# Kernel tuning notes

Hardware: AMD Instinct MI355X
Metric: run time of the kernel (lower is better)

## Reference

```python
import math
import jax, jax.numpy as jnp
import numpy as np

RESO = 64
RADIUS = 1.3
EMB_DIM = 64
NUM_EMB = 512
COMMIT = 0.25
NFP = 4
NFD = 4
SH_DEG = 2
B = 256
_UNITS = 2.0 * RADIUS / (RESO - 1)
STEP = _UNITS / 8.0                      # calc_step_size with factor 4
NINT = int(math.sqrt(3.0) * 2.0 * RADIUS / STEP) - 1   # 871
NSH = (SH_DEG + 1) ** 2                  # 9
MLP_IN = EMB_DIM + 6 * (NFP + NFD)       # 112
MLP_H = 32
MLP_OUT = NSH * 3 + 1                    # 28


def _eval_sh(d):
    # real SH basis, degree 2 -> 9 coeffs, evaluated on unit directions [B,3]
    x, y, z = d[:, 0], d[:, 1], d[:, 2]
    C0 = 0.28209479177387814
    C1 = 0.4886025119029199
    C20, C22, C24 = 1.0925484305920792, 0.31539156525252005, 0.5462742152960396
    return jnp.stack([
        jnp.full_like(x, C0), -C1 * y, C1 * z, -C1 * x,
        C20 * x * y, -C20 * y * z, C22 * (2 * z * z - x * x - y * y),
        -C20 * x * z, C24 * (x * x - y * y)], axis=-1)


def _pe(x, nf):
    # NeRF positional encoding: [N,3] -> [N, 6*nf]
    freqs = (2.0 ** jnp.arange(nf)).astype(x.dtype)
    ang = x[..., None] * freqs                              # [N,3,nf]
    return jnp.concatenate([jnp.sin(ang), jnp.cos(ang)], axis=-1).reshape(x.shape[0], 6 * nf)


def _forward(rays_o, rays_d, data, emb_w, W1, b1, W2, b2, W3, b3):
    rd = rays_d / jnp.linalg.norm(rays_d, axis=1, keepdims=True)
    # ray/AABB intersection, uniform marching (get_intersections)
    inv = 1.0 / rd
    t1 = (-RADIUS - rays_o) * inv
    t2 = (RADIUS - rays_o) * inv
    tnear = jnp.maximum(jnp.max(jnp.minimum(t1, t2), axis=1), 0.0)
    ts = tnear[:, None] + STEP * jnp.arange(NINT, dtype=rays_o.dtype)[None, :]  # [B,NINT]
    pts = rays_o[:, None, :] + ts[..., None] * rd[:, None, :]                   # [B,NINT,3]
    mask = jnp.all(jnp.abs(pts) < RADIUS, axis=-1)                              # [B,NINT]
    pf = pts.reshape(-1, 3)                                                     # [N,3]
    mf = mask.reshape(-1).astype(pf.dtype)                                      # [N]

    # fetch_coarse_interp: trilinear gather from [C,D,H,W] grid (align_corners)
    p = pf / RADIUS
    idx = jnp.clip((p + 1.0) * 0.5 * (RESO - 1), 0.0, RESO - 1)
    i0 = jnp.floor(idx).astype(jnp.int32)
    fr = idx - i0
    i1 = jnp.minimum(i0 + 1, RESO - 1)
    dT = jnp.transpose(data, (1, 2, 3, 0))  # [D,H,W,C]
    g = lambda iz, iy, ix: dT[iz, iy, ix]   # [N,C] gather
    x0, y0, z0 = i0[:, 0], i0[:, 1], i0[:, 2]
    x1, y1, z1 = i1[:, 0], i1[:, 1], i1[:, 2]
    wx, wy, wz = fr[:, 0:1], fr[:, 1:2], fr[:, 2:3]
    c00 = g(z0, y0, x0) * (1 - wx) + g(z0, y0, x1) * wx
    c01 = g(z0, y1, x0) * (1 - wx) + g(z0, y1, x1) * wx
    c10 = g(z1, y0, x0) * (1 - wx) + g(z1, y0, x1) * wx
    c11 = g(z1, y1, x0) * (1 - wx) + g(z1, y1, x1) * wx
    coarse = (c00 * (1 - wy) + c01 * wy) * (1 - wz) + (c10 * (1 - wy) + c11 * wy) * wz  # [N,C]

    # VectorQuantizerEMA forward (outputs are pre-EMA-update, identical in train/eval)
    d2 = (jnp.sum(coarse * coarse, axis=1, keepdims=True)
          + jnp.sum(emb_w * emb_w, axis=1) - 2.0 * coarse @ emb_w.T)  # [N,K]
    code = jnp.argmin(d2, axis=1)
    quant = emb_w[code]                                               # [N,C]
    cnt = jnp.maximum(jnp.sum(mf), 1.0)
    e_loss = jnp.sum(mf[:, None] * (jax.lax.stop_gradient(quant) - coarse) ** 2) / (cnt * EMB_DIM)
    loss = COMMIT * e_loss
    quant_st = coarse + jax.lax.stop_gradient(quant - coarse)
    counts = jax.ops.segment_sum(mf, code, num_segments=NUM_EMB)
    avg = counts / cnt
    perplexity = jnp.exp(-jnp.sum(avg * jnp.log(avg + 1e-10)))

    # world2finecoo + positional encoding
    pcc = pf * (RESO / (2.0 * RADIUS)) + RESO / 2.0
    fine = (pcc - jnp.floor(pcc)) * 2.0 - 1.0
    dirs = jnp.broadcast_to(rd[:, None, :], pts.shape).reshape(-1, 3)
    pe = jnp.concatenate([_pe(fine, NFP), _pe(dirs, NFD)], axis=1)    # [N,48]

    # fine MLP
    h = jax.nn.relu(jnp.concatenate([quant_st, pe], axis=1) @ W1 + b1)
    h = jax.nn.relu(h @ W2 + b2)
    shd = h @ W3 + b3                                                 # [N,28]

    # render: sigma2alpha + SH -> rgb + compositing (masked-out points get 0 weight)
    sigma = (jax.nn.relu(shd[:, -1]) * mf).reshape(B, NINT)
    alpha = 1.0 - jnp.exp(-sigma * STEP)
    Tc = jnp.cumprod(1.0 - alpha + 1e-10, axis=1)
    T = jnp.concatenate([jnp.ones((B, 1), alpha.dtype), Tc[:, :-1]], axis=1)
    w = alpha * T                                                     # abs_light [B,NINT]
    shm = _eval_sh(rd)                                                # [B,9]
    shrgb = shd[:, :-1].reshape(-1, 3, NSH)
    shm_f = jnp.broadcast_to(shm[:, None, :], (B, NINT, NSH)).reshape(-1, NSH)
    rgb_pt = (jnp.sum(shm_f[:, None, :] * shrgb, axis=-1) * mf[:, None]).reshape(B, NINT, 3)
    rgb_pt = jnp.clip(rgb_pt + 0.5, 0.0, 1.0)                         # shrgb2rgb per-sample
    rgb = jnp.sum(w[..., None] * rgb_pt, axis=1) + (1.0 - jnp.sum(w, axis=1, keepdims=True))
    depth = jnp.sum(w * ts, axis=1)
    return rgb, depth, loss, perplexity


def setup_inputs() -> dict:
    key = jax.random.key(0)
    ks = jax.random.split(key, 8)
    rays_o = (jax.random.uniform(ks[0], (B, 3)) * 2.0 - 1.0) * 0.3
    rays_d = jax.random.normal(ks[1], (B, 3))
    data = jax.random.normal(ks[2], (EMB_DIM, RESO, RESO, RESO)) * 0.1
    emb_w = jax.random.normal(ks[3], (NUM_EMB, EMB_DIM))
    W1 = jax.random.normal(ks[4], (MLP_IN, MLP_H)) * (1.0 / math.sqrt(MLP_IN))
    W2 = jax.random.normal(ks[5], (MLP_H, MLP_H)) * (1.0 / math.sqrt(MLP_H))
    W3 = jax.random.normal(ks[6], (MLP_H, MLP_OUT)) * (1.0 / math.sqrt(MLP_H))
    return {
        'rays_o': rays_o, 'rays_d': rays_d, 'grid_id': 0,
        'data': data, 'emb_w': emb_w,
        'W1': W1, 'b1': jnp.zeros((MLP_H,)),
        'W2': W2, 'b2': jnp.zeros((MLP_H,)),
        'W3': W3, 'b3': jnp.zeros((MLP_OUT,)),
    }


def reference(rays_o, rays_d, grid_id, data, emb_w, W1, b1, W2, b2, W3, b3):
    # grid_id is unused in the original forward as well
    return _forward(rays_o, rays_d, data, emb_w, W1, b1, W2, b2, W3, b3)
```

## Files before the change

### kernel.cpp

```cpp
#include <hip/hip_runtime.h>
#include <math.h>

#define NINT 871
#define NB 256
#define NPTS (NB*NINT)
#define NUM_EMB 512
#define EMB_DIM 64
#define RESO 64
#define STEP_F 0.005158730158730159f
#define RADIUS_F 1.3f
#define PCC_SC 24.615384615384617f

#define WS_RD    0
#define WS_TN    768
#define WS_SHM   1024
#define WS_E2    3328
#define WS_CNT   3840
#define WS_ELOSS 4352
#define WS_RGBS  4608

__device__ __forceinline__ float wave_reduce_sum(float v) {
    #pragma unroll
    for (int off = 32; off > 0; off >>= 1) v += __shfl_down(v, off, 64);
    return v;
}

__global__ void setup_kernel(const float* __restrict__ rays_o,
                             const float* __restrict__ rays_d,
                             const float* __restrict__ emb,
                             float* __restrict__ ws) {
    int gid = blockIdx.x * blockDim.x + threadIdx.x;
    if (gid < NB) {
        int r = gid;
        float dx = rays_d[r*3+0], dy = rays_d[r*3+1], dz = rays_d[r*3+2];
        float n = sqrtf(dx*dx + dy*dy + dz*dz);
        float rx = dx/n, ry = dy/n, rz = dz/n;
        ws[WS_RD + r*3+0] = rx; ws[WS_RD + r*3+1] = ry; ws[WS_RD + r*3+2] = rz;
        float ox = rays_o[r*3+0], oy = rays_o[r*3+1], oz = rays_o[r*3+2];
        float ivx = 1.0f/rx, ivy = 1.0f/ry, ivz = 1.0f/rz;
        float mnx = fminf((-RADIUS_F - ox)*ivx, (RADIUS_F - ox)*ivx);
        float mny = fminf((-RADIUS_F - oy)*ivy, (RADIUS_F - oy)*ivy);
        float mnz = fminf((-RADIUS_F - oz)*ivz, (RADIUS_F - oz)*ivz);
        float tn = fmaxf(fmaxf(fmaxf(mnx, mny), mnz), 0.0f);
        ws[WS_TN + r] = tn;
        const float C0=0.28209479177387814f, C1=0.4886025119029199f;
        const float C20=1.0925484305920792f, C22=0.31539156525252005f, C24=0.5462742152960396f;
        float x = rx, y = ry, z = rz;
        float sh[9];
        sh[0] = C0;
        sh[1] = -C1*y;
        sh[2] =  C1*z;
        sh[3] = -C1*x;
        sh[4] =  C20*x*y;
        sh[5] = -C20*y*z;
        sh[6] =  C22*(2.0f*z*z - x*x - y*y);
        sh[7] = -C20*x*z;
        sh[8] =  C24*(x*x - y*y);
        #pragma unroll
        for (int j = 0; j < 9; ++j) ws[WS_SHM + r*9 + j] = sh[j];
    }
    int e = gid - NB;
    if (e >= 0 && e < NUM_EMB) {
        float s = 0.0f;
        #pragma unroll 8
        for (int k = 0; k < EMB_DIM; ++k) { float v = emb[e*EMB_DIM + k]; s += v*v; }
        ws[WS_E2 + e] = s;
    }
}

__global__ __launch_bounds__(64) void point_kernel(
    const float* __restrict__ rays_o,
    const float* __restrict__ data,
    const float* __restrict__ emb,
    const float* __restrict__ W1, const float* __restrict__ b1,
    const float* __restrict__ W2, const float* __restrict__ b2,
    const float* __restrict__ W3, const float* __restrict__ b3,
    float* __restrict__ ws)
{
    __shared__ float smem[64*68];
    __shared__ float lds_e2[64];

    const int tid = threadIdx.x;
    const int ray = blockIdx.y;
    const int s   = blockIdx.x * 64 + tid;
    const bool live = (s < NINT);
    const int  ss = live ? s : (NINT - 1);

    const float rx = ws[WS_RD + ray*3+0];
    const float ry = ws[WS_RD + ray*3+1];
    const float rz = ws[WS_RD + ray*3+2];
    const float tn = ws[WS_TN + ray];
    const float ox = rays_o[ray*3+0], oy = rays_o[ray*3+1], oz = rays_o[ray*3+2];

    const float t  = tn + STEP_F * (float)ss;
    const float px = ox + t*rx, py = oy + t*ry, pz = oz + t*rz;
    const bool mask = live && (fabsf(px) < RADIUS_F) && (fabsf(py) < RADIUS_F) && (fabsf(pz) < RADIUS_F);

    unsigned long long alive = __ballot(mask);
    if (alive == 0ull) {
        if (live) {
            float4 z4; z4.x = 0.0f; z4.y = 0.0f; z4.z = 0.0f; z4.w = 0.0f;
            ((float4*)(ws + WS_RGBS))[ray*NINT + s] = z4;
        }
        return;
    }

    float ix = fminf(fmaxf((px/RADIUS_F + 1.0f)*0.5f*63.0f, 0.0f), 63.0f);
    float iy = fminf(fmaxf((py/RADIUS_F + 1.0f)*0.5f*63.0f, 0.0f), 63.0f);
    float iz = fminf(fmaxf((pz/RADIUS_F + 1.0f)*0.5f*63.0f, 0.0f), 63.0f);
    int x0 = (int)floorf(ix); float wx = ix - (float)x0; int x1 = x0+1 > 63 ? 63 : x0+1;
    int y0 = (int)floorf(iy); float wy = iy - (float)y0; int y1 = y0+1 > 63 ? 63 : y0+1;
    int z0 = (int)floorf(iz); float wz = iz - (float)z0; int z1 = z0+1 > 63 ? 63 : z0+1;
    const int b000 = z0*4096 + y0*64 + x0;
    const int dxo = x1 - x0;
    const int dyo = (y1 - y0)*64;
    const int dzo = (z1 - z0)*4096;
    const float omwx = 1.0f-wx, omwy = 1.0f-wy, omwz = 1.0f-wz;

    float* myrow = smem + tid*68;
    #pragma unroll 4
    for (int c = 0; c < EMB_DIM; ++c) {
        const float* dc = data + c*262144 + b000;
        float v000 = dc[0],       v001 = dc[dxo];
        float v010 = dc[dyo],     v011 = dc[dyo+dxo];
        float v100 = dc[dzo],     v101 = dc[dzo+dxo];
        float v110 = dc[dzo+dyo], v111 = dc[dzo+dyo+dxo];
        float c00 = v000*omwx + v001*wx;
        float c01 = v010*omwx + v011*wx;
        float c10 = v100*omwx + v101*wx;
        float c11 = v110*omwx + v111*wx;
        myrow[c] = (c00*omwy + c01*wy)*omwz + (c10*omwy + c11*wy)*wz;
    }
    __syncthreads();

    float coarse[EMB_DIM];
    #pragma unroll
    for (int k4 = 0; k4 < 16; ++k4) {
        float4 v = *(const float4*)(myrow + k4*4);
        coarse[k4*4+0] = v.x; coarse[k4*4+1] = v.y;
        coarse[k4*4+2] = v.z; coarse[k4*4+3] = v.w;
    }
    __syncthreads();

    float best = 3.4e38f; int bc = 0;
    for (int tile = 0; tile < 8; ++tile) {
        const int cbase = tile*64;
        {
            const float4* src = (const float4*)(emb + cbase*EMB_DIM);
            float4* dst = (float4*)smem;
            #pragma unroll
            for (int i = 0; i < 16; ++i) dst[tid + i*64] = src[tid + i*64];
            lds_e2[tid] = ws[WS_E2 + cbase + tid];
        }
        __syncthreads();

        for (int cq = 0; cq < 16; ++cq) {
            const float* e0 = smem + cq*256;
            float d0 = 0.0f, d1 = 0.0f, d2 = 0.0f, d3 = 0.0f;
            #pragma unroll
            for (int k4 = 0; k4 < 16; ++k4) {
                float4 e0v = *(const float4*)(e0 + k4*4);
                float4 e1v = *(const float4*)(e0 + 64 + k4*4);
                float4 e2v = *(const float4*)(e0 + 128 + k4*4);
                float4 e3v = *(const float4*)(e0 + 192 + k4*4);
                float c0v = coarse[4*k4+0], c1v = coarse[4*k4+1];
                float c2v = coarse[4*k4+2], c3v = coarse[4*k4+3];
                d0 = fmaf(c0v, e0v.x, d0); d0 = fmaf(c1v, e0v.y, d0);
                d0 = fmaf(c2v, e0v.z, d0); d0 = fmaf(c3v, e0v.w, d0);
                d1 = fmaf(c0v, e1v.x, d1); d1 = fmaf(c1v, e1v.y, d1);
                d1 = fmaf(c2v, e1v.z, d1); d1 = fmaf(c3v, e1v.w, d1);
                d2 = fmaf(c0v, e2v.x, d2); d2 = fmaf(c1v, e2v.y, d2);
                d2 = fmaf(c2v, e2v.z, d2); d2 = fmaf(c3v, e2v.w, d2);
                d3 = fmaf(c0v, e3v.x, d3); d3 = fmaf(c1v, e3v.y, d3);
                d3 = fmaf(c2v, e3v.z, d3); d3 = fmaf(c3v, e3v.w, d3);
            }
            float s0 = lds_e2[cq*4+0] - 2.0f*d0;
            float s1 = lds_e2[cq*4+1] - 2.0f*d1;
            float s2 = lds_e2[cq*4+2] - 2.0f*d2;
            float s3 = lds_e2[cq*4+3] - 2.0f*d3;
            int cb = cbase + cq*4;
            if (s0 < best) { best = s0; bc = cb + 0; }
            if (s1 < best) { best = s1; bc = cb + 1; }
            if (s2 < best) { best = s2; bc = cb + 2; }
            if (s3 < best) { best = s3; bc = cb + 3; }
        }
        __syncthreads();
    }

    {
        float* hist = smem;
        #pragma unroll
        for (int i = 0; i < 8; ++i) hist[tid + i*64] = 0.0f;
        __syncthreads();
        if (mask) atomicAdd(&hist[bc], 1.0f);
        __syncthreads();
        #pragma unroll
        for (int i = 0; i < 8; ++i) {
            float h = hist[tid + i*64];
            if (h != 0.0f) atomicAdd(&ws[WS_CNT + tid + i*64], h);
        }
    }

    float h1[32];
    #pragma unroll
    for (int j = 0; j < 32; ++j) h1[j] = b1[j];

    float diff2 = 0.0f;
    {
        const float4* eq4 = (const float4*)(emb + bc*EMB_DIM);
        #pragma unroll
        for (int k4 = 0; k4 < 16; ++k4) {
            float4 q4 = eq4[k4];
            float q[4] = {q4.x, q4.y, q4.z, q4.w};
            #pragma unroll
            for (int u = 0; u < 4; ++u) {
                int k = k4*4 + u;
                float d  = q[u] - coarse[k];
                diff2 += d*d;
                float xv = coarse[k] + d;
                #pragma unroll
                for (int j = 0; j < 32; ++j) h1[j] = fmaf(xv, W1[k*32 + j], h1[j]);
            }
        }
    }
    float el = mask ? diff2 : 0.0f;
    el = wave_reduce_sum(el);
    if (tid == 0 && el != 0.0f) atomicAdd(&ws[WS_ELOSS], el);

    {
        float fx = px*PCC_SC + 32.0f; fx = (fx - floorf(fx))*2.0f - 1.0f;
        float fy = py*PCC_SC + 32.0f; fy = (fy - floorf(fy))*2.0f - 1.0f;
        float fz = pz*PCC_SC + 32.0f; fz = (fz - floorf(fz))*2.0f - 1.0f;
        float fv[3] = {fx, fy, fz};
        float dv[3] = {rx, ry, rz};
        #pragma unroll
        for (int a = 0; a < 3; ++a) {
            #pragma unroll
            for (int f = 0; f < 4; ++f) {
                float angf = fv[a] * (float)(1 << f);
                float angd = dv[a] * (float)(1 << f);
                float sf = sinf(angf), cf = cosf(angf);
                float sd = sinf(angd), cd = cosf(angd);
                int rowS = 64 + a*8 + f;
                int rowC = rowS + 4;
                int rowSD = 88 + a*8 + f;
                int rowCD = rowSD + 4;
                #pragma unroll
                for (int j = 0; j < 32; ++j) {
                    h1[j] = fmaf(sf, W1[rowS*32 + j], h1[j]);
                    h1[j] = fmaf(cf, W1[rowC*32 + j], h1[j]);
                    h1[j] = fmaf(sd, W1[rowSD*32 + j], h1[j]);
                    h1[j] = fmaf(cd, W1[rowCD*32 + j], h1[j]);
                }
            }
        }
    }
    #pragma unroll
    for (int j = 0; j < 32; ++j) h1[j] = fmaxf(h1[j], 0.0f);

    float h2[32];
    #pragma unroll
    for (int j = 0; j < 32; ++j) h2[j] = b2[j];
    #pragma unroll
    for (int k = 0; k < 32; ++k) {
        float hv = h1[k];
        #pragma unroll
        for (int j = 0; j < 32; ++j) h2[j] = fmaf(hv, W2[k*32 + j], h2[j]);
    }
    #pragma unroll
    for (int j = 0; j < 32; ++j) h2[j] = fmaxf(h2[j], 0.0f);

    float shd[28];
    #pragma unroll
    for (int j = 0; j < 28; ++j) shd[j] = b3[j];
    #pragma unroll
    for (int k = 0; k < 32; ++k) {
        float hv = h2[k];
        #pragma unroll
        for (int j = 0; j < 28; ++j) shd[j] = fmaf(hv, W3[k*28 + j], shd[j]);
    }

    const float mf = mask ? 1.0f : 0.0f;
    float sigma = fmaxf(shd[27], 0.0f) * mf;

    float shm_[9];
    #pragma unroll
    for (int j = 0; j < 9; ++j) shm_[j] = ws[WS_SHM + ray*9 + j];

    float rgb[3];
    #pragma unroll
    for (int c = 0; c < 3; ++c) {
        float acc = 0.0f;
        #pragma unroll
        for (int j = 0; j < 9; ++j) acc = fmaf(shm_[j], shd[c*9 + j], acc);
        rgb[c] = fminf(fmaxf(acc*mf + 0.5f, 0.0f), 1.0f);
    }

    if (live) {
        float4 o4; o4.x = rgb[0]; o4.y = rgb[1]; o4.z = rgb[2]; o4.w = sigma;
        ((float4*)(ws + WS_RGBS))[ray*NINT + s] = o4;
    }
}

__global__ void composite_kernel(const float* __restrict__ ws, float* __restrict__ out) {
    const int lane = threadIdx.x & 63;
    const int wid  = threadIdx.x >> 6;
    const int r = blockIdx.x * (blockDim.x >> 6) + wid;
    if (r >= NB) return;

    const float tn = ws[WS_TN + r];
    const float4* rs = ((const float4*)(ws + WS_RGBS)) + r*NINT;

    const int s0 = lane * 14;
    float T = 1.0f, c0 = 0.0f, c1 = 0.0f, c2 = 0.0f, dep = 0.0f, wsum = 0.0f;
    #pragma unroll 2
    for (int i = 0; i < 14; ++i) {
        int s = s0 + i;
        if (s < NINT) {
            float4 v = rs[s];
            float alpha = 1.0f - expf(-v.w * STEP_F);
            float w = alpha * T;
            c0 += w * v.x; c1 += w * v.y; c2 += w * v.z;
            dep  += w * (tn + STEP_F * (float)s);
            wsum += w;
            T *= (1.0f - alpha + 1e-10f);
        }
    }

    float inc = T;
    #pragma unroll
    for (int off = 1; off < 64; off <<= 1) {
        float o = __shfl_up(inc, off, 64);
        if (lane >= off) inc *= o;
    }
    float excl = __shfl_up(inc, 1, 64);
    if (lane == 0) excl = 1.0f;

    c0 *= excl; c1 *= excl; c2 *= excl; dep *= excl; wsum *= excl;
    c0 = wave_reduce_sum(c0);
    c1 = wave_reduce_sum(c1);
    c2 = wave_reduce_sum(c2);
    dep = wave_reduce_sum(dep);
    wsum = wave_reduce_sum(wsum);

    if (lane == 0) {
        float bg = 1.0f - wsum;
        out[r*3+0] = c0 + bg;
        out[r*3+1] = c1 + bg;
        out[r*3+2] = c2 + bg;
        out[768 + r] = dep;
    }
}

__global__ void finalize_kernel(const float* __restrict__ ws, float* __restrict__ out) {
    __shared__ float red[512];
    int t = threadIdx.x;
    float c = ws[WS_CNT + t];
    red[t] = c;
    __syncthreads();
    #pragma unroll
    for (int off = 256; off > 0; off >>= 1) {
        if (t < off) red[t] += red[t + off];
        __syncthreads();
    }
    float cnt = fmaxf(red[0], 1.0f);
    __syncthreads();
    float avg = c / cnt;
    red[t] = avg * logf(avg + 1e-10f);
    __syncthreads();
    #pragma unroll
    for (int off = 256; off > 0; off >>= 1) {
        if (t < off) red[t] += red[t + off];
        __syncthreads();
    }
    if (t == 0) {
        out[1024] = 0.25f * ws[WS_ELOSS] / (cnt * 64.0f);
        out[1025] = expf(-red[0]);
    }
}

extern "C" void kernel_launch(void* const* d_in, const int* in_sizes, int n_in,
                              void* d_out, int out_size, void* d_ws, size_t ws_size,
                              hipStream_t stream) {
    const float* rays_o = (const float*)d_in[0];
    const float* rays_d = (const float*)d_in[1];
    const float* data   = (const float*)d_in[3];
    const float* emb    = (const float*)d_in[4];
    const float* W1 = (const float*)d_in[5];
    const float* b1 = (const float*)d_in[6];
    const float* W2 = (const float*)d_in[7];
    const float* b2 = (const float*)d_in[8];
    const float* W3 = (const float*)d_in[9];
    const float* b3 = (const float*)d_in[10];
    float* ws  = (float*)d_ws;
    float* out = (float*)d_out;

    hipMemsetAsync(ws + WS_CNT, 0, (NUM_EMB + 1) * sizeof(float), stream);

    setup_kernel<<<3, 256, 0, stream>>>(rays_o, rays_d, emb, ws);

    dim3 gB((NINT + 63) / 64, NB);
    point_kernel<<<gB, 64, 0, stream>>>(rays_o, data, emb, W1, b1, W2, b2, W3, b3, ws);

    composite_kernel<<<64, 256, 0, stream>>>(ws, out);
    finalize_kernel<<<1, 512, 0, stream>>>(ws, out);
}
```

Baseline: 385.9 us.

## Process two sample points per thread to reuse codebook LDS reads

Each thread now handles two samples (A and B) along the ray, so every codebook vector read from shared memory feeds two dot products instead of one. The codebook tile shrinks to 32 entries across 16 tiles, and the grid halves along the sample axis. This cuts LDS traffic per FMA and per-block setup cost. In exchange it doubles the register footprint (two 64-float coarse arrays), which can lower occupancy or cause spills, and gives each block a coarser unit of work.

```diff
diff --git a/kernel.cpp b/kernel.cpp
--- a/kernel.cpp
+++ b/kernel.cpp
@@ -77,14 +77,18 @@
     const float* __restrict__ W3, const float* __restrict__ b3,
     float* __restrict__ ws)
 {
-    __shared__ float smem[64*68];
-    __shared__ float lds_e2[64];
+    __shared__ float cls[128*68];
+    __shared__ float lds_emb[32*64];
+    __shared__ float lds_e2[32];
 
     const int tid = threadIdx.x;
     const int ray = blockIdx.y;
-    const int s   = blockIdx.x * 64 + tid;
-    const bool live = (s < NINT);
-    const int  ss = live ? s : (NINT - 1);
+    const int sA  = blockIdx.x * 128 + tid;
+    const int sB  = sA + 64;
+    const bool liveA = (sA < NINT);
+    const bool liveB = (sB < NINT);
+    const int ssA = liveA ? sA : (NINT - 1);
+    const int ssB = liveB ? sB : (NINT - 1);
 
     const float rx = ws[WS_RD + ray*3+0];
     const float ry = ws[WS_RD + ray*3+1];
@@ -92,107 +96,152 @@
     const float tn = ws[WS_TN + ray];
     const float ox = rays_o[ray*3+0], oy = rays_o[ray*3+1], oz = rays_o[ray*3+2];
 
-    const float t  = tn + STEP_F * (float)ss;
-    const float px = ox + t*rx, py = oy + t*ry, pz = oz + t*rz;
-    const bool mask = live && (fabsf(px) < RADIUS_F) && (fabsf(py) < RADIUS_F) && (fabsf(pz) < RADIUS_F);
-
-    unsigned long long alive = __ballot(mask);
+    const float tA = tn + STEP_F * (float)ssA;
+    const float tB = tn + STEP_F * (float)ssB;
+    const float pxA = ox + tA*rx, pyA = oy + tA*ry, pzA = oz + tA*rz;
+    const float pxB = ox + tB*rx, pyB = oy + tB*ry, pzB = oz + tB*rz;
+    const bool maskA = liveA && (fabsf(pxA) < RADIUS_F) && (fabsf(pyA) < RADIUS_F) && (fabsf(pzA) < RADIUS_F);
+    const bool maskB = liveB && (fabsf(pxB) < RADIUS_F) && (fabsf(pyB) < RADIUS_F) && (fabsf(pzB) < RADIUS_F);
+
+    unsigned long long alive = __ballot(maskA || maskB);
     if (alive == 0ull) {
-        if (live) {
-            float4 z4; z4.x = 0.0f; z4.y = 0.0f; z4.z = 0.0f; z4.w = 0.0f;
-            ((float4*)(ws + WS_RGBS))[ray*NINT + s] = z4;
-        }
+        float4 z4; z4.x = 0.0f; z4.y = 0.0f; z4.z = 0.0f; z4.w = 0.0f;
+        if (liveA) ((float4*)(ws + WS_RGBS))[ray*NINT + sA] = z4;
+        if (liveB) ((float4*)(ws + WS_RGBS))[ray*NINT + sB] = z4;
         return;
     }
 
-    float ix = fminf(fmaxf((px/RADIUS_F + 1.0f)*0.5f*63.0f, 0.0f), 63.0f);
-    float iy = fminf(fmaxf((py/RADIUS_F + 1.0f)*0.5f*63.0f, 0.0f), 63.0f);
-    float iz = fminf(fmaxf((pz/RADIUS_F + 1.0f)*0.5f*63.0f, 0.0f), 63.0f);
-    int x0 = (int)floorf(ix); float wx = ix - (float)x0; int x1 = x0+1 > 63 ? 63 : x0+1;
-    int y0 = (int)floorf(iy); float wy = iy - (float)y0; int y1 = y0+1 > 63 ? 63 : y0+1;
-    int z0 = (int)floorf(iz); float wz = iz - (float)z0; int z1 = z0+1 > 63 ? 63 : z0+1;
-    const int b000 = z0*4096 + y0*64 + x0;
-    const int dxo = x1 - x0;
-    const int dyo = (y1 - y0)*64;
-    const int dzo = (z1 - z0)*4096;
-    const float omwx = 1.0f-wx, omwy = 1.0f-wy, omwz = 1.0f-wz;
-
-    float* myrow = smem + tid*68;
+    float ixA = fminf(fmaxf((pxA/RADIUS_F + 1.0f)*0.5f*63.0f, 0.0f), 63.0f);
+    float iyA = fminf(fmaxf((pyA/RADIUS_F + 1.0f)*0.5f*63.0f, 0.0f), 63.0f);
+    float izA = fminf(fmaxf((pzA/RADIUS_F + 1.0f)*0.5f*63.0f, 0.0f), 63.0f);
+    int x0A = (int)floorf(ixA); float wxA = ixA - (float)x0A; int x1A = x0A+1 > 63 ? 63 : x0A+1;
+    int y0A = (int)floorf(iyA); float wyA = iyA - (float)y0A; int y1A = y0A+1 > 63 ? 63 : y0A+1;
+    int z0A = (int)floorf(izA); float wzA = izA - (float)z0A; int z1A = z0A+1 > 63 ? 63 : z0A+1;
+    const int b000A = z0A*4096 + y0A*64 + x0A;
+    const int dxoA = x1A - x0A;
+    const int dyoA = (y1A - y0A)*64;
+    const int dzoA = (z1A - z0A)*4096;
+    const float omwxA = 1.0f-wxA, omwyA = 1.0f-wyA, omwzA = 1.0f-wzA;
+
+    float ixB = fminf(fmaxf((pxB/RADIUS_F + 1.0f)*0.5f*63.0f, 0.0f), 63.0f);
+    float iyB = fminf(fmaxf((pyB/RADIUS_F + 1.0f)*0.5f*63.0f, 0.0f), 63.0f);
+    float izB = fminf(fmaxf((pzB/RADIUS_F + 1.0f)*0.5f*63.0f, 0.0f), 63.0f);
+    int x0B = (int)floorf(ixB); float wxB = ixB - (float)x0B; int x1B = x0B+1 > 63 ? 63 : x0B+1;
+    int y0B = (int)floorf(iyB); float wyB = iyB - (float)y0B; int y1B = y0B+1 > 63 ? 63 : y0B+1;
+    int z0B = (int)floorf(izB); float wzB = izB - (float)z0B; int z1B = z0B+1 > 63 ? 63 : z0B+1;
+    const int b000B = z0B*4096 + y0B*64 + x0B;
+    const int dxoB = x1B - x0B;
+    const int dyoB = (y1B - y0B)*64;
+    const int dzoB = (z1B - z0B)*4096;
+    const float omwxB = 1.0f-wxB, omwyB = 1.0f-wyB, omwzB = 1.0f-wzB;
+
+    float* rowA = cls + tid*68;
+    float* rowB = cls + (64 + tid)*68;
     #pragma unroll 4
     for (int c = 0; c < EMB_DIM; ++c) {
-        const float* dc = data + c*262144 + b000;
-        float v000 = dc[0],       v001 = dc[dxo];
-        float v010 = dc[dyo],     v011 = dc[dyo+dxo];
-        float v100 = dc[dzo],     v101 = dc[dzo+dxo];
-        float v110 = dc[dzo+dyo], v111 = dc[dzo+dyo+dxo];
-        float c00 = v000*omwx + v001*wx;
-        float c01 = v010*omwx + v011*wx;
-        float c10 = v100*omwx + v101*wx;
-        float c11 = v110*omwx + v111*wx;
-        myrow[c] = (c00*omwy + c01*wy)*omwz + (c10*omwy + c11*wy)*wz;
+        {
+            const float* dc = data + c*262144 + b000A;
+            float v000 = dc[0],         v001 = dc[dxoA];
+            float v010 = dc[dyoA],      v011 = dc[dyoA+dxoA];
+            float v100 = dc[dzoA],      v101 = dc[dzoA+dxoA];
+            float v110 = dc[dzoA+dyoA], v111 = dc[dzoA+dyoA+dxoA];
+            float c00 = v000*omwxA + v001*wxA;
+            float c01 = v010*omwxA + v011*wxA;
+            float c10 = v100*omwxA + v101*wxA;
+            float c11 = v110*omwxA + v111*wxA;
+            rowA[c] = (c00*omwyA + c01*wyA)*omwzA + (c10*omwyA + c11*wyA)*wzA;
+        }
+        {
+            const float* dc = data + c*262144 + b000B;
+            float v000 = dc[0],         v001 = dc[dxoB];
+            float v010 = dc[dyoB],      v011 = dc[dyoB+dxoB];
+            float v100 = dc[dzoB],      v101 = dc[dzoB+dxoB];
+            float v110 = dc[dzoB+dyoB], v111 = dc[dzoB+dyoB+dxoB];
+            float c00 = v000*omwxB + v001*wxB;
+            float c01 = v010*omwxB + v011*wxB;
+            float c10 = v100*omwxB + v101*wxB;
+            float c11 = v110*omwxB + v111*wxB;
+            rowB[c] = (c00*omwyB + c01*wyB)*omwzB + (c10*omwyB + c11*wyB)*wzB;
+        }
     }
     __syncthreads();
 
-    float coarse[EMB_DIM];
+    float cA[EMB_DIM], cB[EMB_DIM];
     #pragma unroll
     for (int k4 = 0; k4 < 16; ++k4) {
-        float4 v = *(const float4*)(myrow + k4*4);
-        coarse[k4*4+0] = v.x; coarse[k4*4+1] = v.y;
-        coarse[k4*4+2] = v.z; coarse[k4*4+3] = v.w;
-    }
-    __syncthreads();
-
-    float best = 3.4e38f; int bc = 0;
-    for (int tile = 0; tile < 8; ++tile) {
-        const int cbase = tile*64;
+        float4 va = *(const float4*)(rowA + k4*4);
+        cA[k4*4+0] = va.x; cA[k4*4+1] = va.y; cA[k4*4+2] = va.z; cA[k4*4+3] = va.w;
+        float4 vb = *(const float4*)(rowB + k4*4);
+        cB[k4*4+0] = vb.x; cB[k4*4+1] = vb.y; cB[k4*4+2] = vb.z; cB[k4*4+3] = vb.w;
+    }
+
+    float bestA = 3.4e38f, bestB = 3.4e38f; int bcA = 0, bcB = 0;
+    for (int tile = 0; tile < 16; ++tile) {
+        const int cbase = tile*32;
         {
             const float4* src = (const float4*)(emb + cbase*EMB_DIM);
-            float4* dst = (float4*)smem;
-            #pragma unroll
-            for (int i = 0; i < 16; ++i) dst[tid + i*64] = src[tid + i*64];
-            lds_e2[tid] = ws[WS_E2 + cbase + tid];
+            float4* dst = (float4*)lds_emb;
+            #pragma unroll
+            for (int i = 0; i < 8; ++i) dst[tid + i*64] = src[tid + i*64];
+            if (tid < 32) lds_e2[tid] = ws[WS_E2 + cbase + tid];
         }
         __syncthreads();
 
-        for (int cq = 0; cq < 16; ++cq) {
-            const float* e0 = smem + cq*256;
-            float d0 = 0.0f, d1 = 0.0f, d2 = 0.0f, d3 = 0.0f;
+        for (int cq = 0; cq < 8; ++cq) {
+            const float* e0 = lds_emb + cq*256;
+            float dA0 = 0.0f, dA1 = 0.0f, dA2 = 0.0f, dA3 = 0.0f;
+            float dB0 = 0.0f, dB1 = 0.0f, dB2 = 0.0f, dB3 = 0.0f;
             #pragma unroll
             for (int k4 = 0; k4 < 16; ++k4) {
                 float4 e0v = *(const float4*)(e0 + k4*4);
                 float4 e1v = *(const float4*)(e0 + 64 + k4*4);
                 float4 e2v = *(const float4*)(e0 + 128 + k4*4);
                 float4 e3v = *(const float4*)(e0 + 192 + k4*4);
-                float c0v = coarse[4*k4+0], c1v = coarse[4*k4+1];
-                float c2v = coarse[4*k4+2], c3v = coarse[4*k4+3];
-                d0 = fmaf(c0v, e0v.x, d0); d0 = fmaf(c1v, e0v.y, d0);
-                d0 = fmaf(c2v, e0v.z, d0); d0 = fmaf(c3v, e0v.w, d0);
-                d1 = fmaf(c0v, e1v.x, d1); d1 = fmaf(c1v, e1v.y, d1);
-                d1 = fmaf(c2v, e1v.z, d1); d1 = fmaf(c3v, e1v.w, d1);
-                d2 = fmaf(c0v, e2v.x, d2); d2 = fmaf(c1v, e2v.y, d2);
-                d2 = fmaf(c2v, e2v.z, d2); d2 = fmaf(c3v, e2v.w, d2);
-                d3 = fmaf(c0v, e3v.x, d3); d3 = fmaf(c1v, e3v.y, d3);
-                d3 = fmaf(c2v, e3v.z, d3); d3 = fmaf(c3v, e3v.w, d3);
+                float a0 = cA[4*k4+0], a1 = cA[4*k4+1], a2 = cA[4*k4+2], a3 = cA[4*k4+3];
+                float b0 = cB[4*k4+0], b1v = cB[4*k4+1], b2v = cB[4*k4+2], b3v = cB[4*k4+3];
+                dA0 = fmaf(a0, e0v.x, dA0); dA0 = fmaf(a1, e0v.y, dA0);
+                dA0 = fmaf(a2, e0v.z, dA0); dA0 = fmaf(a3, e0v.w, dA0);
+                dA1 = fmaf(a0, e1v.x, dA1); dA1 = fmaf(a1, e1v.y, dA1);
+                dA1 = fmaf(a2, e1v.z, dA1); dA1 = fmaf(a3, e1v.w, dA1);
+                dA2 = fmaf(a0, e2v.x, dA2); dA2 = fmaf(a1, e2v.y, dA2);
+                dA2 = fmaf(a2, e2v.z, dA2); dA2 = fmaf(a3, e2v.w, dA2);
+                dA3 = fmaf(a0, e3v.x, dA3); dA3 = fmaf(a1, e3v.y, dA3);
+                dA3 = fmaf(a2, e3v.z, dA3); dA3 = fmaf(a3, e3v.w, dA3);
+                dB0 = fmaf(b0, e0v.x, dB0); dB0 = fmaf(b1v, e0v.y, dB0);
+                dB0 = fmaf(b2v, e0v.z, dB0); dB0 = fmaf(b3v, e0v.w, dB0);
+                dB1 = fmaf(b0, e1v.x, dB1); dB1 = fmaf(b1v, e1v.y, dB1);
+                dB1 = fmaf(b2v, e1v.z, dB1); dB1 = fmaf(b3v, e1v.w, dB1);
+                dB2 = fmaf(b0, e2v.x, dB2); dB2 = fmaf(b1v, e2v.y, dB2);
+                dB2 = fmaf(b2v, e2v.z, dB2); dB2 = fmaf(b3v, e2v.w, dB2);
+                dB3 = fmaf(b0, e3v.x, dB3); dB3 = fmaf(b1v, e3v.y, dB3);
+                dB3 = fmaf(b2v, e3v.z, dB3); dB3 = fmaf(b3v, e3v.w, dB3);
             }
-            float s0 = lds_e2[cq*4+0] - 2.0f*d0;
-            float s1 = lds_e2[cq*4+1] - 2.0f*d1;
-            float s2 = lds_e2[cq*4+2] - 2.0f*d2;
-            float s3 = lds_e2[cq*4+3] - 2.0f*d3;
+            float q0 = lds_e2[cq*4+0], q1 = lds_e2[cq*4+1];
+            float q2 = lds_e2[cq*4+2], q3 = lds_e2[cq*4+3];
             int cb = cbase + cq*4;
-            if (s0 < best) { best = s0; bc = cb + 0; }
-            if (s1 < best) { best = s1; bc = cb + 1; }
-            if (s2 < best) { best = s2; bc = cb + 2; }
-            if (s3 < best) { best = s3; bc = cb + 3; }
+            float sA0 = q0 - 2.0f*dA0, sA1 = q1 - 2.0f*dA1;
+            float sA2 = q2 - 2.0f*dA2, sA3 = q3 - 2.0f*dA3;
+            if (sA0 < bestA) { bestA = sA0; bcA = cb + 0; }
+            if (sA1 < bestA) { bestA = sA1; bcA = cb + 1; }
+            if (sA2 < bestA) { bestA = sA2; bcA = cb + 2; }
+            if (sA3 < bestA) { bestA = sA3; bcA = cb + 3; }
+            float sB0 = q0 - 2.0f*dB0, sB1 = q1 - 2.0f*dB1;
+            float sB2 = q2 - 2.0f*dB2, sB3 = q3 - 2.0f*dB3;
+            if (sB0 < bestB) { bestB = sB0; bcB = cb + 0; }
+            if (sB1 < bestB) { bestB = sB1; bcB = cb + 1; }
+            if (sB2 < bestB) { bestB = sB2; bcB = cb + 2; }
+            if (sB3 < bestB) { bestB = sB3; bcB = cb + 3; }
         }
         __syncthreads();
     }
 
     {
-        float* hist = smem;
+        float* hist = lds_emb;
         #pragma unroll
         for (int i = 0; i < 8; ++i) hist[tid + i*64] = 0.0f;
         __syncthreads();
-        if (mask) atomicAdd(&hist[bc], 1.0f);
+        if (maskA) atomicAdd(&hist[bcA], 1.0f);
+        if (maskB) atomicAdd(&hist[bcB], 1.0f);
         __syncthreads();
         #pragma unroll
         for (int i = 0; i < 8; ++i) {
@@ -201,104 +250,200 @@
         }
     }
 
-    float h1[32];
-    #pragma unroll
-    for (int j = 0; j < 32; ++j) h1[j] = b1[j];
-
-    float diff2 = 0.0f;
-    {
-        const float4* eq4 = (const float4*)(emb + bc*EMB_DIM);
-        #pragma unroll
-        for (int k4 = 0; k4 < 16; ++k4) {
-            float4 q4 = eq4[k4];
-            float q[4] = {q4.x, q4.y, q4.z, q4.w};
-            #pragma unroll
-            for (int u = 0; u < 4; ++u) {
-                int k = k4*4 + u;
-                float d  = q[u] - coarse[k];
-                diff2 += d*d;
-                float xv = coarse[k] + d;
-                #pragma unroll
-                for (int j = 0; j < 32; ++j) h1[j] = fmaf(xv, W1[k*32 + j], h1[j]);
-            }
-        }
-    }
-    float el = mask ? diff2 : 0.0f;
-    el = wave_reduce_sum(el);
-    if (tid == 0 && el != 0.0f) atomicAdd(&ws[WS_ELOSS], el);
-
-    {
-        float fx = px*PCC_SC + 32.0f; fx = (fx - floorf(fx))*2.0f - 1.0f;
-        float fy = py*PCC_SC + 32.0f; fy = (fy - floorf(fy))*2.0f - 1.0f;
-        float fz = pz*PCC_SC + 32.0f; fz = (fz - floorf(fz))*2.0f - 1.0f;
-        float fv[3] = {fx, fy, fz};
-        float dv[3] = {rx, ry, rz};
-        #pragma unroll
-        for (int a = 0; a < 3; ++a) {
-            #pragma unroll
-            for (int f = 0; f < 4; ++f) {
-                float angf = fv[a] * (float)(1 << f);
-                float angd = dv[a] * (float)(1 << f);
-                float sf = sinf(angf), cf = cosf(angf);
-                float sd = sinf(angd), cd = cosf(angd);
-                int rowS = 64 + a*8 + f;
-                int rowC = rowS + 4;
-                int rowSD = 88 + a*8 + f;
-                int rowCD = rowSD + 4;
-                #pragma unroll
-                for (int j = 0; j < 32; ++j) {
-                    h1[j] = fmaf(sf, W1[rowS*32 + j], h1[j]);
-                    h1[j] = fmaf(cf, W1[rowC*32 + j], h1[j]);
-                    h1[j] = fmaf(sd, W1[rowSD*32 + j], h1[j]);
-                    h1[j] = fmaf(cd, W1[rowCD*32 + j], h1[j]);
-                }
-            }
-        }
-    }
-    #pragma unroll
-    for (int j = 0; j < 32; ++j) h1[j] = fmaxf(h1[j], 0.0f);
-
-    float h2[32];
-    #pragma unroll
-    for (int j = 0; j < 32; ++j) h2[j] = b2[j];
-    #pragma unroll
-    for (int k = 0; k < 32; ++k) {
-        float hv = h1[k];
-        #pragma unroll
-        for (int j = 0; j < 32; ++j) h2[j] = fmaf(hv, W2[k*32 + j], h2[j]);
-    }
-    #pragma unroll
-    for (int j = 0; j < 32; ++j) h2[j] = fmaxf(h2[j], 0.0f);
-
-    float shd[28];
-    #pragma unroll
-    for (int j = 0; j < 28; ++j) shd[j] = b3[j];
-    #pragma unroll
-    for (int k = 0; k < 32; ++k) {
-        float hv = h2[k];
-        #pragma unroll
-        for (int j = 0; j < 28; ++j) shd[j] = fmaf(hv, W3[k*28 + j], shd[j]);
-    }
-
-    const float mf = mask ? 1.0f : 0.0f;
-    float sigma = fmaxf(shd[27], 0.0f) * mf;
-
     float shm_[9];
     #pragma unroll
     for (int j = 0; j < 9; ++j) shm_[j] = ws[WS_SHM + ray*9 + j];
 
-    float rgb[3];
-    #pragma unroll
-    for (int c = 0; c < 3; ++c) {
-        float acc = 0.0f;
-        #pragma unroll
-        for (int j = 0; j < 9; ++j) acc = fmaf(shm_[j], shd[c*9 + j], acc);
-        rgb[c] = fminf(fmaxf(acc*mf + 0.5f, 0.0f), 1.0f);
-    }
-
-    if (live) {
-        float4 o4; o4.x = rgb[0]; o4.y = rgb[1]; o4.z = rgb[2]; o4.w = sigma;
-        ((float4*)(ws + WS_RGBS))[ray*NINT + s] = o4;
+    {
+        float h1[32];
+        #pragma unroll
+        for (int j = 0; j < 32; ++j) h1[j] = b1[j];
+
+        float diff2 = 0.0f;
+        {
+            const float4* eq4 = (const float4*)(emb + bcA*EMB_DIM);
+            #pragma unroll
+            for (int k4 = 0; k4 < 16; ++k4) {
+                float4 q4 = eq4[k4];
+                float q[4] = {q4.x, q4.y, q4.z, q4.w};
+                #pragma unroll
+                for (int u = 0; u < 4; ++u) {
+                    int k = k4*4 + u;
+                    float d  = q[u] - cA[k];
+                    diff2 += d*d;
+                    float xv = cA[k] + d;
+                    #pragma unroll
+                    for (int j = 0; j < 32; ++j) h1[j] = fmaf(xv, W1[k*32 + j], h1[j]);
+                }
+            }
+        }
+        float el = maskA ? diff2 : 0.0f;
+        el = wave_reduce_sum(el);
+        if (tid == 0 && el != 0.0f) atomicAdd(&ws[WS_ELOSS], el);
+
+        {
+            float fx = pxA*PCC_SC + 32.0f; fx = (fx - floorf(fx))*2.0f - 1.0f;
+            float fy = pyA*PCC_SC + 32.0f; fy = (fy - floorf(fy))*2.0f - 1.0f;
+            float fz = pzA*PCC_SC + 32.0f; fz = (fz - floorf(fz))*2.0f - 1.0f;
+            float fv[3] = {fx, fy, fz};
+            float dv[3] = {rx, ry, rz};
+            #pragma unroll
+            for (int a = 0; a < 3; ++a) {
+                #pragma unroll
+                for (int f = 0; f < 4; ++f) {
+                    float angf = fv[a] * (float)(1 << f);
+                    float angd = dv[a] * (float)(1 << f);
+                    float sf = sinf(angf), cf = cosf(angf);
+                    float sd = sinf(angd), cd = cosf(angd);
+                    int rowS = 64 + a*8 + f;
+                    int rowC = rowS + 4;
+                    int rowSD = 88 + a*8 + f;
+                    int rowCD = rowSD + 4;
+                    #pragma unroll
+                    for (int j = 0; j < 32; ++j) {
+                        h1[j] = fmaf(sf, W1[rowS*32 + j], h1[j]);
+                        h1[j] = fmaf(cf, W1[rowC*32 + j], h1[j]);
+                        h1[j] = fmaf(sd, W1[rowSD*32 + j], h1[j]);
+                        h1[j] = fmaf(cd, W1[rowCD*32 + j], h1[j]);
+                    }
+                }
+            }
+        }
+        #pragma unroll
+        for (int j = 0; j < 32; ++j) h1[j] = fmaxf(h1[j], 0.0f);
+
+        float h2[32];
+        #pragma unroll
+        for (int j = 0; j < 32; ++j) h2[j] = b2[j];
+        #pragma unroll
+        for (int k = 0; k < 32; ++k) {
+            float hv = h1[k];
+            #pragma unroll
+            for (int j = 0; j < 32; ++j) h2[j] = fmaf(hv, W2[k*32 + j], h2[j]);
+        }
+        #pragma unroll
+        for (int j = 0; j < 32; ++j) h2[j] = fmaxf(h2[j], 0.0f);
+
+        float shd[28];
+        #pragma unroll
+        for (int j = 0; j < 28; ++j) shd[j] = b3[j];
+        #pragma unroll
+        for (int k = 0; k < 32; ++k) {
+            float hv = h2[k];
+            #pragma unroll
+            for (int j = 0; j < 28; ++j) shd[j] = fmaf(hv, W3[k*28 + j], shd[j]);
+        }
+
+        const float mf = maskA ? 1.0f : 0.0f;
+        float sigma = fmaxf(shd[27], 0.0f) * mf;
+        float rgb[3];
+        #pragma unroll
+        for (int c = 0; c < 3; ++c) {
+            float acc = 0.0f;
+            #pragma unroll
+            for (int j = 0; j < 9; ++j) acc = fmaf(shm_[j], shd[c*9 + j], acc);
+            rgb[c] = fminf(fmaxf(acc*mf + 0.5f, 0.0f), 1.0f);
+        }
+        if (liveA) {
+            float4 o4; o4.x = rgb[0]; o4.y = rgb[1]; o4.z = rgb[2]; o4.w = sigma;
+            ((float4*)(ws + WS_RGBS))[ray*NINT + sA] = o4;
+        }
+    }
+
+    {
+        float h1[32];
+        #pragma unroll
+        for (int j = 0; j < 32; ++j) h1[j] = b1[j];
+
+        float diff2 = 0.0f;
+        {
+            const float4* eq4 = (const float4*)(emb + bcB*EMB_DIM);
+            #pragma unroll
+            for (int k4 = 0; k4 < 16; ++k4) {
+                float4 q4 = eq4[k4];
+                float q[4] = {q4.x, q4.y, q4.z, q4.w};
+                #pragma unroll
+                for (int u = 0; u < 4; ++u) {
+                    int k = k4*4 + u;
+                    float d  = q[u] - cB[k];
+                    diff2 += d*d;
+                    float xv = cB[k] + d;
+                    #pragma unroll
+                    for (int j = 0; j < 32; ++j) h1[j] = fmaf(xv, W1[k*32 + j], h1[j]);
+                }
+            }
+        }
+        float el = maskB ? diff2 : 0.0f;
+        el = wave_reduce_sum(el);
+        if (tid == 0 && el != 0.0f) atomicAdd(&ws[WS_ELOSS], el);
+
+        {
+            float fx = pxB*PCC_SC + 32.0f; fx = (fx - floorf(fx))*2.0f - 1.0f;
+            float fy = pyB*PCC_SC + 32.0f; fy = (fy - floorf(fy))*2.0f - 1.0f;
+            float fz = pzB*PCC_SC + 32.0f; fz = (fz - floorf(fz))*2.0f - 1.0f;
+            float fv[3] = {fx, fy, fz};
+            float dv[3] = {rx, ry, rz};
+            #pragma unroll
+            for (int a = 0; a < 3; ++a) {
+                #pragma unroll
+                for (int f = 0; f < 4; ++f) {
+                    float angf = fv[a] * (float)(1 << f);
+                    float angd = dv[a] * (float)(1 << f);
+                    float sf = sinf(angf), cf = cosf(angf);
+                    float sd = sinf(angd), cd = cosf(angd);
+                    int rowS = 64 + a*8 + f;
+                    int rowC = rowS + 4;
+                    int rowSD = 88 + a*8 + f;
+                    int rowCD = rowSD + 4;
+                    #pragma unroll
+                    for (int j = 0; j < 32; ++j) {
+                        h1[j] = fmaf(sf, W1[rowS*32 + j], h1[j]);
+                        h1[j] = fmaf(cf, W1[rowC*32 + j], h1[j]);
+                        h1[j] = fmaf(sd, W1[rowSD*32 + j], h1[j]);
+                        h1[j] = fmaf(cd, W1[rowCD*32 + j], h1[j]);
+                    }
+                }
+            }
+        }
+        #pragma unroll
+        for (int j = 0; j < 32; ++j) h1[j] = fmaxf(h1[j], 0.0f);
+
+        float h2[32];
+        #pragma unroll
+        for (int j = 0; j < 32; ++j) h2[j] = b2[j];
+        #pragma unroll
+        for (int k = 0; k < 32; ++k) {
+            float hv = h1[k];
+            #pragma unroll
+            for (int j = 0; j < 32; ++j) h2[j] = fmaf(hv, W2[k*32 + j], h2[j]);
+        }
+        #pragma unroll
+        for (int j = 0; j < 32; ++j) h2[j] = fmaxf(h2[j], 0.0f);
+
+        float shd[28];
+        #pragma unroll
+        for (int j = 0; j < 28; ++j) shd[j] = b3[j];
+        #pragma unroll
+        for (int k = 0; k < 32; ++k) {
+            float hv = h2[k];
+            #pragma unroll
+            for (int j = 0; j < 28; ++j) shd[j] = fmaf(hv, W3[k*28 + j], shd[j]);
+        }
+
+        const float mf = maskB ? 1.0f : 0.0f;
+        float sigma = fmaxf(shd[27], 0.0f) * mf;
+        float rgb[3];
+        #pragma unroll
+        for (int c = 0; c < 3; ++c) {
+            float acc = 0.0f;
+            #pragma unroll
+            for (int j = 0; j < 9; ++j) acc = fmaf(shm_[j], shd[c*9 + j], acc);
+            rgb[c] = fminf(fmaxf(acc*mf + 0.5f, 0.0f), 1.0f);
+        }
+        if (liveB) {
+            float4 o4; o4.x = rgb[0]; o4.y = rgb[1]; o4.z = rgb[2]; o4.w = sigma;
+            ((float4*)(ws + WS_RGBS))[ray*NINT + sB] = o4;
+        }
     }
 }
 
@@ -399,7 +544,7 @@
 
     setup_kernel<<<3, 256, 0, stream>>>(rays_o, rays_d, emb, ws);
 
-    dim3 gB((NINT + 63) / 64, NB);
+    dim3 gB((NINT + 127) / 128, NB);
     point_kernel<<<gB, 64, 0, stream>>>(rays_o, data, emb, W1, b1, W2, b2, W3, b3, ws);
 
     composite_kernel<<<64, 256, 0, stream>>>(ws, out);
```

New measurement: 960.1 us. 2.49x slower.
